# Performance work log

Measured on AMD Instinct MI355X. Metric: run time of the kernel, lower is better.

The kernel has to match this reference:

```python
import jax, jax.numpy as jnp
import numpy as np

D_MODEL = 1024
N_HEADS = 16
D_K = D_MODEL // N_HEADS


def setup_inputs() -> dict:
    key = jax.random.key(0)
    kx, kq, kk, kv, ko = jax.random.split(key, 5)
    s = 1.0 / np.sqrt(D_MODEL)
    return {
        "x": jax.random.normal(kx, (4, 2048, D_MODEL), dtype=jnp.float32),
        "W_q": jax.random.normal(kq, (D_MODEL, D_MODEL), dtype=jnp.float32) * s,
        "W_k": jax.random.normal(kk, (D_MODEL, D_MODEL), dtype=jnp.float32) * s,
        "W_v": jax.random.normal(kv, (D_MODEL, D_MODEL), dtype=jnp.float32) * s,
        "W_o": jax.random.normal(ko, (D_MODEL, D_MODEL), dtype=jnp.float32) * s,
    }


def reference(x, W_q, W_k, W_v, W_o):
    B, S, _ = x.shape
    # torch nn.Linear computes x @ W.T; our W_* stored as [out, in]-equivalent square,
    # use plain x @ W (equivalent parameterization for a random weight).
    def split_heads(t):  # [B,S,D] -> [B,H,S,d_k]
        return t.reshape(B, S, N_HEADS, D_K).transpose(0, 2, 1, 3)

    Q = split_heads(x @ W_q)
    K = split_heads(x @ W_k)
    V = split_heads(x @ W_v)
    scale = 1.0 / np.sqrt(D_K).astype(np.float32)
    scores = jnp.einsum('bhqd,bhkd->bhqk', Q, K) * scale  # [B,H,S,S]
    causal_mask = jnp.tril(jnp.ones((S, S), dtype=bool))  # True = keep
    scores = jnp.where(causal_mask, scores, jnp.float32(-jnp.inf))
    attn = jax.nn.softmax(scores, axis=-1)
    out = jnp.einsum('bhqk,bhkd->bhqd', attn, V)  # [B,H,S,d_k]
    out = out.transpose(0, 2, 1, 3).reshape(B, S, D_MODEL)
    return out @ W_o
```

## Files before the change

kernel.cpp:

```cpp
#include <hip/hip_runtime.h>
#include <hip/hip_bf16.h>
#include <stdint.h>

#define B_SZ 4
#define SEQ 2048
#define DM 1024
#define NH 16
#define DK 64
#define BH (B_SZ * NH)
#define M_TOT (B_SZ * SEQ)

typedef unsigned short u16;
typedef u16 u16x8 __attribute__((ext_vector_type(8)));
typedef __bf16 bf16x8 __attribute__((ext_vector_type(8)));
typedef float f32x4 __attribute__((ext_vector_type(4)));

__device__ __forceinline__ u16 f2bf(float f) {
    return __builtin_bit_cast(u16, (__bf16)f);
}

__device__ __forceinline__ u16 f2bf_trunc(float f) {
    union { float f; uint32_t u; } v; v.f = f;
    return (u16)(v.u >> 16);
}

__device__ __forceinline__ f32x4 mfma16(u16x8 a, u16x8 b, f32x4 c) {
    return __builtin_amdgcn_mfma_f32_16x16x32_bf16(
        __builtin_bit_cast(bf16x8, a), __builtin_bit_cast(bf16x8, b), c, 0, 0, 0);
}

__device__ __forceinline__ void gload16_lds(const void* g, void* l) {
    __builtin_amdgcn_global_load_lds(
        (const __attribute__((address_space(1))) void*)(uintptr_t)g,
        (__attribute__((address_space(3))) void*)(uintptr_t)l, 16, 0, 0);
}

__global__ void cvt_bf16_kernel(const float* __restrict__ in, u16* __restrict__ out, int n4) {
    int i = blockIdx.x * blockDim.x + threadIdx.x;
    if (i < n4) {
        float4 v = ((const float4*)in)[i];
        ushort4 o;
        o.x = f2bf(v.x); o.y = f2bf(v.y); o.z = f2bf(v.z); o.w = f2bf(v.w);
        ((ushort4*)out)[i] = o;
    }
}

__global__ void transpose_w_kernel(const float* __restrict__ W0, const float* __restrict__ W1,
                                   u16* __restrict__ Wt) {
    __shared__ u16 tile[32][33];
    int bx = blockIdx.x, by = blockIdx.y, z = blockIdx.z;
    const float* W = z ? W1 : W0;
    u16* Wd = Wt + (size_t)z * DM * DM;
    int t = threadIdx.x;
    for (int i = 0; i < 4; i++) {
        int idx = t + i * 256;
        int r = idx >> 5, c = idx & 31;
        tile[r][c] = f2bf(W[(by * 32 + r) * DM + bx * 32 + c]);
    }
    __syncthreads();
    for (int i = 0; i < 4; i++) {
        int idx = t + i * 256;
        int r2 = idx >> 5, c2 = idx & 31;
        Wd[(bx * 32 + r2) * DM + by * 32 + c2] = tile[c2][r2];
    }
}

template <int AFP32, int MODE>
__global__ __launch_bounds__(256, 3) void gemm128(
    const void* __restrict__ Ain, const u16* __restrict__ Bt,
    void* __restrict__ C0p, void* __restrict__ C1p, float scale0) {
    __shared__ u16 As[128][32];
    __shared__ u16 Bs[128][32];
    const int K = DM;
    int m0 = blockIdx.x * 128;
    int n0 = blockIdx.y * 128;
    int tid = threadIdx.x;
    int lane = tid & 63, wave = tid >> 6;
    int quad = lane >> 4, l15 = lane & 15;
    int wm = wave >> 1, wn = wave & 1;

    f32x4 acc[4][4];
    for (int i = 0; i < 4; i++)
        for (int j = 0; j < 4; j++) acc[i][j] = f32x4{0.f, 0.f, 0.f, 0.f};

    int rS = lane >> 2;
    int cS = (lane & 3) * 8;

    for (int k0 = 0; k0 < K; k0 += 32) {
        __syncthreads();
        if (AFP32) {
            const float* A = (const float*)Ain;
            for (int i = 0; i < 4; i++) {
                int idx = tid + i * 256;
                int r = idx >> 3, c = (idx & 7) * 4;
                float4 v = *(const float4*)(&A[(size_t)(m0 + r) * K + k0 + c]);
                ushort4 o;
                o.x = f2bf(v.x); o.y = f2bf(v.y); o.z = f2bf(v.z); o.w = f2bf(v.w);
                *(ushort4*)(&As[r][c]) = o;
            }
        } else {
            const u16* A = (const u16*)Ain;
            const u16* ga = &A[(size_t)(m0 + wave * 32 + rS) * K + k0 + cS];
            gload16_lds(ga, &As[wave * 32][0]);
            gload16_lds(ga + (size_t)16 * K, &As[wave * 32 + 16][0]);
        }
        {
            const u16* gb = &Bt[(size_t)(n0 + wave * 32 + rS) * K + k0 + cS];
            gload16_lds(gb, &Bs[wave * 32][0]);
            gload16_lds(gb + (size_t)16 * K, &Bs[wave * 32 + 16][0]);
        }
        __syncthreads();
        u16x8 af[4], bfv[4];
        for (int mt = 0; mt < 4; mt++)
            af[mt] = *(const u16x8*)(&As[wm * 64 + mt * 16 + l15][quad * 8]);
        for (int nt = 0; nt < 4; nt++)
            bfv[nt] = *(const u16x8*)(&Bs[wn * 64 + nt * 16 + l15][quad * 8]);
        for (int mt = 0; mt < 4; mt++)
            for (int nt = 0; nt < 4; nt++)
                acc[mt][nt] = mfma16(af[mt], bfv[nt], acc[mt][nt]);
    }

    if constexpr (MODE == 2) {
        __shared__ u16 Ct[4][64][68];
        #pragma unroll
        for (int mt = 0; mt < 4; mt++)
            #pragma unroll
            for (int nt = 0; nt < 4; nt++)
                #pragma unroll
                for (int r = 0; r < 4; r++) {
                    int mp = mt * 16 + quad * 4 + r;
                    int np = nt * 16 + l15;
                    Ct[wave][np][mp] = f2bf(acc[mt][nt][r]);
                }
        __syncthreads();
        int bb = m0 >> 11;
        int hh = (n0 + wn * 64) >> 6;
        int s_base = (m0 & 2047) + wm * 64;
        u16* Cv = (u16*)C0p;
        #pragma unroll
        for (int c = 0; c < 8; c++) {
            int np = (lane >> 3) + c * 8;
            int mp = (lane & 7) * 8;
            ushort4 lo = *(const ushort4*)(&Ct[wave][np][mp]);
            ushort4 hi = *(const ushort4*)(&Ct[wave][np][mp + 4]);
            u16x8 v;
            v[0] = lo.x; v[1] = lo.y; v[2] = lo.z; v[3] = lo.w;
            v[4] = hi.x; v[5] = hi.y; v[6] = hi.z; v[7] = hi.w;
            size_t addr = ((size_t)(bb * NH + hh) * DK + np) * SEQ + s_base + mp;
            *(u16x8*)(&Cv[addr]) = v;
        }
    } else {
        for (int mt = 0; mt < 4; mt++)
            for (int nt = 0; nt < 4; nt++)
                for (int r = 0; r < 4; r++) {
                    int m = m0 + wm * 64 + mt * 16 + quad * 4 + r;
                    int n = n0 + wn * 64 + nt * 16 + l15;
                    float v = acc[mt][nt][r];
                    if (MODE == 0) {
                        v *= (n < 1024) ? scale0 : 1.0f;
                        u16* C = (n < 1024) ? (u16*)C0p : (u16*)C1p;
                        int ne = n & 1023;
                        int b = m >> 11, s = m & 2047;
                        int h = ne >> 6, d = ne & 63;
                        C[(((size_t)(b * NH + h) * SEQ) + s) * DK + d] = f2bf(v);
                    } else {
                        ((float*)C0p)[(size_t)m * DM + n] = v;
                    }
                }
    }
}

__global__ __launch_bounds__(256, 3) void attn_kernel(
    const u16* __restrict__ Qb, const u16* __restrict__ Kb,
    const u16* __restrict__ Vtb, u16* __restrict__ AOb) {
    __shared__ u16 Kl[2][64][64];
    __shared__ u16 Vl[2][64][64];
    __shared__ u16 Pl[4][32][64];

    int bh = blockIdx.x;
    int qs = 15 - blockIdx.y;
    int q0 = qs * 128;
    int tid = threadIdx.x, lane = tid & 63, wave = tid >> 6;
    int quad = lane >> 4, l15 = lane & 15;
    int b = bh >> 4, h = bh & 15;

    const u16* Qg = Qb + (size_t)bh * SEQ * DK;
    const u16* Kg = Kb + (size_t)bh * SEQ * DK;
    const u16* Vg = Vtb + (size_t)bh * DK * SEQ;

    int rw = lane >> 3;
    int gsw = (lane & 7) ^ rw;
    int sw8 = l15 & 7;
    u16* Pw = &Pl[wave][0][0];

    u16x8 aq[2][2];
    for (int g = 0; g < 2; g++)
        for (int kc = 0; kc < 2; kc++)
            aq[g][kc] = *(const u16x8*)(
                &Qg[(size_t)(q0 + wave * 32 + g * 16 + l15) * DK + kc * 32 + quad * 8]);

    float lsum[2][4];
    f32x4 O[2][4];
    for (int g = 0; g < 2; g++)
        for (int r = 0; r < 4; r++) lsum[g][r] = 0.f;
    for (int g = 0; g < 2; g++)
        for (int nt = 0; nt < 4; nt++) O[g][nt] = f32x4{0.f, 0.f, 0.f, 0.f};

    {
        const u16* gk = &Kg[(size_t)(wave * 16 + rw) * DK + gsw * 8];
        gload16_lds(gk, &Kl[0][wave * 16][0]);
        gload16_lds(gk + 8 * DK, &Kl[0][wave * 16 + 8][0]);
        const u16* gv = &Vg[(size_t)(wave * 16 + rw) * SEQ + gsw * 8];
        gload16_lds(gv, &Vl[0][wave * 16][0]);
        gload16_lds(gv + 8 * SEQ, &Vl[0][wave * 16 + 8][0]);
    }
    __syncthreads();

    int nkt = 2 * qs + 2;
    int lastkt = 2 * qs + (wave >> 1);
    int buf = 0;
    for (int kt = 0; kt < nkt; kt++) {
        if (kt + 1 < nkt) {
            int k0n = (kt + 1) * 64;
            const u16* gk = &Kg[(size_t)(k0n + wave * 16 + rw) * DK + gsw * 8];
            gload16_lds(gk, &Kl[buf ^ 1][wave * 16][0]);
            gload16_lds(gk + 8 * DK, &Kl[buf ^ 1][wave * 16 + 8][0]);
            const u16* gv = &Vg[(size_t)(wave * 16 + rw) * SEQ + k0n + gsw * 8];
            gload16_lds(gv, &Vl[buf ^ 1][wave * 16][0]);
            gload16_lds(gv + 8 * SEQ, &Vl[buf ^ 1][wave * 16 + 8][0]);
        }

        if (kt <= lastkt) {
            bool diag = (kt == lastkt);
            f32x4 sc[2][4];
            __builtin_amdgcn_s_setprio(1);
            #pragma unroll
            for (int nt = 0; nt < 4; nt++) {
                const u16* kr = &Kl[buf][nt * 16 + l15][0];
                u16x8 b0 = *(const u16x8*)(kr + (quad ^ sw8) * 8);
                u16x8 b1 = *(const u16x8*)(kr + ((4 + quad) ^ sw8) * 8);
                #pragma unroll
                for (int g = 0; g < 2; g++) {
                    f32x4 z = f32x4{0.f, 0.f, 0.f, 0.f};
                    z = mfma16(aq[g][0], b0, z);
                    z = mfma16(aq[g][1], b1, z);
                    sc[g][nt] = z;
                }
            }
            __builtin_amdgcn_s_setprio(0);
            #pragma unroll
            for (int g = 0; g < 2; g++) {
                if (diag) {
                    #pragma unroll
                    for (int nt = 0; nt < 4; nt++)
                        #pragma unroll
                        for (int r = 0; r < 4; r++) {
                            int qq = q0 + wave * 32 + g * 16 + quad * 4 + r;
                            int kk = kt * 64 + nt * 16 + l15;
                            float e = exp2f(sc[g][nt][r]);
                            float pv = (kk <= qq) ? e : 0.f;
                            sc[g][nt][r] = pv;
                            lsum[g][r] += pv;
                        }
                } else {
                    #pragma unroll
                    for (int nt = 0; nt < 4; nt++)
                        #pragma unroll
                        for (int r = 0; r < 4; r++) {
                            float pv = exp2f(sc[g][nt][r]);
                            sc[g][nt][r] = pv;
                            lsum[g][r] += pv;
                        }
                }
                #pragma unroll
                for (int nt = 0; nt < 4; nt++)
                    #pragma unroll
                    for (int r = 0; r < 4; r++) {
                        int prow = g * 16 + quad * 4 + r;
                        int pcol = nt * 16 + l15;
                        int scol = (((pcol >> 3) ^ (prow & 7)) << 3) | (pcol & 7);
                        Pw[prow * 64 + scol] = f2bf_trunc(sc[g][nt][r]);
                    }
            }
            u16x8 ap[2][2];
            #pragma unroll
            for (int g = 0; g < 2; g++)
                #pragma unroll
                for (int kc = 0; kc < 2; kc++)
                    ap[g][kc] = *(const u16x8*)(
                        &Pw[(g * 16 + l15) * 64 + (((kc * 4 + quad) ^ sw8) << 3)]);
            __builtin_amdgcn_s_setprio(1);
            #pragma unroll
            for (int nt = 0; nt < 4; nt++) {
                const u16* vr = &Vl[buf][nt * 16 + l15][0];
                u16x8 b0 = *(const u16x8*)(vr + (quad ^ sw8) * 8);
                u16x8 b1 = *(const u16x8*)(vr + ((4 + quad) ^ sw8) * 8);
                #pragma unroll
                for (int g = 0; g < 2; g++) {
                    O[g][nt] = mfma16(ap[g][0], b0, O[g][nt]);
                    O[g][nt] = mfma16(ap[g][1], b1, O[g][nt]);
                }
            }
            __builtin_amdgcn_s_setprio(0);
        }
        __syncthreads();
        buf ^= 1;
    }

    #pragma unroll
    for (int g = 0; g < 2; g++)
        #pragma unroll
        for (int r = 0; r < 4; r++) {
            float s = lsum[g][r];
            for (int off = 1; off < 16; off <<= 1) s += __shfl_xor(s, off, 64);
            float inv = 1.0f / s;
            int q = q0 + wave * 32 + g * 16 + quad * 4 + r;
            #pragma unroll
            for (int nt = 0; nt < 4; nt++) {
                int d = nt * 16 + l15;
                AOb[((size_t)(b * SEQ + q)) * DM + h * DK + d] = f2bf(O[g][nt][r] * inv);
            }
        }
}

extern "C" void kernel_launch(void* const* d_in, const int* in_sizes, int n_in,
                              void* d_out, int out_size, void* d_ws, size_t ws_size,
                              hipStream_t stream) {
    const float* x = (const float*)d_in[0];
    const float* Wq = (const float*)d_in[1];
    const float* Wk = (const float*)d_in[2];
    const float* Wv = (const float*)d_in[3];
    const float* Wo = (const float*)d_in[4];
    float* out = (float*)d_out;

    const size_t HALF = (size_t)M_TOT * DM * 2;
    char* S0 = (char*)d_ws;
    char* S1 = (char*)d_ws + HALF;
    char* D0 = (char*)d_out;
    char* D1 = (char*)d_out + HALF;

    u16* xb  = (u16*)S0;
    u16* Qb  = (u16*)S1;
    u16* Kb  = (u16*)D1;
    u16* Vt  = (u16*)D0;
    u16* AOb = (u16*)S0;
    u16* wqk = (u16*)D0;
    u16* wvt = (u16*)S0;
    u16* wot = (u16*)S1;

    const float cscale = 0.125f * 1.44269504088896f;
    dim3 tg2(32, 32, 2);
    dim3 tg1(32, 32, 1);
    dim3 gg(M_TOT / 128, DM / 128);

    int n4 = M_TOT * DM / 4;
    cvt_bf16_kernel<<<n4 / 256, 256, 0, stream>>>(x, xb, n4);

    transpose_w_kernel<<<tg2, 256, 0, stream>>>(Wq, Wk, wqk);
    dim3 gqk(M_TOT / 128, 2048 / 128);
    gemm128<0, 0><<<gqk, 256, 0, stream>>>(xb, wqk, (void*)Qb, (void*)Kb, cscale);

    transpose_w_kernel<<<tg1, 256, 0, stream>>>(Wv, Wv, wvt);
    gemm128<1, 2><<<gg, 256, 0, stream>>>(x, wvt, (void*)Vt, (void*)Vt, 1.0f);

    dim3 ag(BH, 16);
    attn_kernel<<<ag, 256, 0, stream>>>(Qb, Kb, Vt, AOb);

    transpose_w_kernel<<<tg1, 256, 0, stream>>>(Wo, Wo, wot);
    gemm128<0, 1><<<gg, 256, 0, stream>>>(AOb, wot, (void*)out, (void*)out, 1.0f);
}
```

Baseline: 268.5 us.

## Double-buffer GEMM tiles with async LDS loads, XOR swizzle and grid swizzle

Rewrites the projection GEMM main loop to use a K-tile of 64 with two LDS buffers, prefetching two tiles ahead through direct global-to-LDS loads gated by vmcnt waits. The fp32 A operand is now staged raw into LDS and converted to bf16 on read, rather than converted through registers during the copy. XOR swizzles are added to the LDS layout to avoid bank conflicts, block indices are remapped for L2 locality, and MFMA sections get raised priority. The larger LDS footprint lowers occupancy (launch bounds drop to 1 or 2 blocks), and the hand-written waitcnt values must match the exact number of issued loads.

```diff
diff --git a/kernel.cpp b/kernel.cpp
--- a/kernel.cpp
+++ b/kernel.cpp
@@ -65,59 +65,140 @@
     }
 }
 
+template <int AFP32>
+__device__ __forceinline__ void stage_tile(const void* Ag, const u16* Btg,
+                                           char* Apart, char* Bpart, int buf, int kst,
+                                           int m0, int n0, int wave, int lane) {
+    const int K = DM;
+    {
+        int rw = lane >> 3, slot = lane & 7;
+        int gsw = slot ^ rw;
+        u16* Bb = (u16*)(Bpart + buf * (128 * 64 * 2));
+        #pragma unroll
+        for (int c = 0; c < 4; c++) {
+            int r0 = wave * 32 + c * 8;
+            gload16_lds(Btg + (size_t)(n0 + r0 + rw) * K + kst + gsw * 8, Bb + r0 * 64);
+        }
+    }
+    if constexpr (AFP32) {
+        int rw = lane >> 4, slot = lane & 15;
+        float* Ab = (float*)(Apart + buf * (128 * 64 * 4));
+        const float* Af = (const float*)Ag;
+        #pragma unroll
+        for (int c = 0; c < 8; c++) {
+            int r0 = wave * 32 + c * 4;
+            int gsw = slot ^ ((c * 4 + rw) & 15);
+            gload16_lds(Af + (size_t)(m0 + r0 + rw) * K + kst + gsw * 4, Ab + r0 * 64);
+        }
+    } else {
+        int rw = lane >> 3, slot = lane & 7;
+        int gsw = slot ^ rw;
+        u16* Ab = (u16*)(Apart + buf * (128 * 64 * 2));
+        const u16* Au = (const u16*)Ag;
+        #pragma unroll
+        for (int c = 0; c < 4; c++) {
+            int r0 = wave * 32 + c * 8;
+            gload16_lds(Au + (size_t)(m0 + r0 + rw) * K + kst + gsw * 8, Ab + r0 * 64);
+        }
+    }
+}
+
 template <int AFP32, int MODE>
-__global__ __launch_bounds__(256, 3) void gemm128(
+__global__ __launch_bounds__(256, AFP32 ? 1 : 2) void gemm128(
     const void* __restrict__ Ain, const u16* __restrict__ Bt,
     void* __restrict__ C0p, void* __restrict__ C1p, float scale0) {
-    __shared__ u16 As[128][32];
-    __shared__ u16 Bs[128][32];
-    const int K = DM;
-    int m0 = blockIdx.x * 128;
-    int n0 = blockIdx.y * 128;
+    constexpr int ABY = AFP32 ? 128 * 64 * 4 : 128 * 64 * 2;
+    constexpr int BBY = 128 * 64 * 2;
+    constexpr int NT = DM / 64;
+    __shared__ __align__(16) char smem[2 * ABY + 2 * BBY];
+    char* Apart = smem;
+    char* Bpart = smem + 2 * ABY;
+
+    int gm = gridDim.x;
+    int lin = blockIdx.x + blockIdx.y * gm;
+    int cpx = (gm * gridDim.y) >> 3;
+    int swz = (lin & 7) * cpx + (lin >> 3);
+    int m0 = (swz % gm) * 128;
+    int n0 = (swz / gm) * 128;
+
     int tid = threadIdx.x;
     int lane = tid & 63, wave = tid >> 6;
     int quad = lane >> 4, l15 = lane & 15;
     int wm = wave >> 1, wn = wave & 1;
 
     f32x4 acc[4][4];
+    #pragma unroll
     for (int i = 0; i < 4; i++)
+        #pragma unroll
         for (int j = 0; j < 4; j++) acc[i][j] = f32x4{0.f, 0.f, 0.f, 0.f};
 
-    int rS = lane >> 2;
-    int cS = (lane & 3) * 8;
-
-    for (int k0 = 0; k0 < K; k0 += 32) {
-        __syncthreads();
-        if (AFP32) {
-            const float* A = (const float*)Ain;
-            for (int i = 0; i < 4; i++) {
-                int idx = tid + i * 256;
-                int r = idx >> 3, c = (idx & 7) * 4;
-                float4 v = *(const float4*)(&A[(size_t)(m0 + r) * K + k0 + c]);
-                ushort4 o;
-                o.x = f2bf(v.x); o.y = f2bf(v.y); o.z = f2bf(v.z); o.w = f2bf(v.w);
-                *(ushort4*)(&As[r][c]) = o;
+    stage_tile<AFP32>(Ain, Bt, Apart, Bpart, 0, 0, m0, n0, wave, lane);
+    stage_tile<AFP32>(Ain, Bt, Apart, Bpart, 1, 64, m0, n0, wave, lane);
+
+    for (int t = 0; t < NT; ++t) {
+        int buf = t & 1;
+        if constexpr (AFP32)
+            asm volatile("s_waitcnt vmcnt(12)" ::: "memory");
+        else
+            asm volatile("s_waitcnt vmcnt(8)" ::: "memory");
+        __builtin_amdgcn_s_barrier();
+
+        u16x8 afr[4][2], bfr[4][2];
+        {
+            const u16* Bb = (const u16*)(Bpart + buf * BBY);
+            #pragma unroll
+            for (int nt = 0; nt < 4; nt++) {
+                const u16* rp = Bb + (wn * 64 + nt * 16 + l15) * 64;
+                int sw = l15 & 7;
+                bfr[nt][0] = *(const u16x8*)(rp + ((quad ^ sw) << 3));
+                bfr[nt][1] = *(const u16x8*)(rp + (((4 + quad) ^ sw) << 3));
+            }
+        }
+        if constexpr (AFP32) {
+            const float* Ab = (const float*)(Apart + buf * ABY);
+            #pragma unroll
+            for (int mt = 0; mt < 4; mt++) {
+                const float* rp = Ab + (wm * 64 + mt * 16 + l15) * 64;
+                #pragma unroll
+                for (int ks = 0; ks < 2; ks++) {
+                    int g0 = ks * 8 + quad * 2;
+                    f32x4 v0 = *(const f32x4*)(rp + ((g0 ^ l15) << 2));
+                    f32x4 v1 = *(const f32x4*)(rp + (((g0 + 1) ^ l15) << 2));
+                    u16x8 tt;
+                    tt[0] = f2bf(v0[0]); tt[1] = f2bf(v0[1]);
+                    tt[2] = f2bf(v0[2]); tt[3] = f2bf(v0[3]);
+                    tt[4] = f2bf(v1[0]); tt[5] = f2bf(v1[1]);
+                    tt[6] = f2bf(v1[2]); tt[7] = f2bf(v1[3]);
+                    afr[mt][ks] = tt;
+                }
             }
         } else {
-            const u16* A = (const u16*)Ain;
-            const u16* ga = &A[(size_t)(m0 + wave * 32 + rS) * K + k0 + cS];
-            gload16_lds(ga, &As[wave * 32][0]);
-            gload16_lds(ga + (size_t)16 * K, &As[wave * 32 + 16][0]);
-        }
-        {
-            const u16* gb = &Bt[(size_t)(n0 + wave * 32 + rS) * K + k0 + cS];
-            gload16_lds(gb, &Bs[wave * 32][0]);
-            gload16_lds(gb + (size_t)16 * K, &Bs[wave * 32 + 16][0]);
-        }
-        __syncthreads();
-        u16x8 af[4], bfv[4];
+            const u16* Ab = (const u16*)(Apart + buf * ABY);
+            #pragma unroll
+            for (int mt = 0; mt < 4; mt++) {
+                const u16* rp = Ab + (wm * 64 + mt * 16 + l15) * 64;
+                int sw = l15 & 7;
+                afr[mt][0] = *(const u16x8*)(rp + ((quad ^ sw) << 3));
+                afr[mt][1] = *(const u16x8*)(rp + (((4 + quad) ^ sw) << 3));
+            }
+        }
+        asm volatile("s_waitcnt lgkmcnt(0)" ::: "memory");
+        __builtin_amdgcn_sched_barrier(0);
+        __builtin_amdgcn_s_barrier();
+
+        int t2 = t + 2;
+        if (t2 > NT - 1) t2 = NT - 1;
+        stage_tile<AFP32>(Ain, Bt, Apart, Bpart, buf, t2 * 64, m0, n0, wave, lane);
+
+        __builtin_amdgcn_s_setprio(1);
+        #pragma unroll
         for (int mt = 0; mt < 4; mt++)
-            af[mt] = *(const u16x8*)(&As[wm * 64 + mt * 16 + l15][quad * 8]);
-        for (int nt = 0; nt < 4; nt++)
-            bfv[nt] = *(const u16x8*)(&Bs[wn * 64 + nt * 16 + l15][quad * 8]);
-        for (int mt = 0; mt < 4; mt++)
-            for (int nt = 0; nt < 4; nt++)
-                acc[mt][nt] = mfma16(af[mt], bfv[nt], acc[mt][nt]);
+            #pragma unroll
+            for (int nt = 0; nt < 4; nt++) {
+                acc[mt][nt] = mfma16(afr[mt][0], bfr[nt][0], acc[mt][nt]);
+                acc[mt][nt] = mfma16(afr[mt][1], bfr[nt][1], acc[mt][nt]);
+            }
+        __builtin_amdgcn_s_setprio(0);
     }
 
     if constexpr (MODE == 2) {
@@ -150,8 +231,11 @@
             *(u16x8*)(&Cv[addr]) = v;
         }
     } else {
+        #pragma unroll
         for (int mt = 0; mt < 4; mt++)
+            #pragma unroll
             for (int nt = 0; nt < 4; nt++)
+                #pragma unroll
                 for (int r = 0; r < 4; r++) {
                     int m = m0 + wm * 64 + mt * 16 + quad * 4 + r;
                     int n = n0 + wn * 64 + nt * 16 + l15;
```

New measurement: 277.9 us. 1.03x slower.

## Add double-buffered 256x128 GEMM with XOR-swizzled LDS for QK and output projections

Applied to the files above, without the earlier changes.

Replaces the 128x128 single-buffered GEMM used for the QK and output projections with a 512-thread 256x128 tile kernel. It uses a BK=64 double-buffered global-to-LDS pipeline, XOR-swizzled LDS rows to avoid bank conflicts, grouped block ordering for L2 reuse and raised wave priority around the MFMA loop. The V projection keeps the old design in a separate specialized kernel. The aim is to hide memory latency and raise MFMA utilization, at the cost of more LDS per block and lower occupancy.

```diff
diff --git a/kernel.cpp b/kernel.cpp
--- a/kernel.cpp
+++ b/kernel.cpp
@@ -65,10 +65,117 @@
     }
 }
 
-template <int AFP32, int MODE>
-__global__ __launch_bounds__(256, 3) void gemm128(
-    const void* __restrict__ Ain, const u16* __restrict__ Bt,
+template <int MODE>
+__global__ __launch_bounds__(512, 2) void gemm256(
+    const u16* __restrict__ Ain, const u16* __restrict__ Bt,
     void* __restrict__ C0p, void* __restrict__ C1p, float scale0) {
+    constexpr int NT = DM / 64;
+    __shared__ __align__(16) u16 As[2 * 256 * 64];
+    __shared__ __align__(16) u16 Bs[2 * 128 * 64];
+
+    int gm = gridDim.x;
+    int lin = blockIdx.x + blockIdx.y * gm;
+    int cpx = (gm * gridDim.y) >> 3;
+    int swz = (lin & 7) * cpx + (lin >> 3);
+    int m0 = (swz % gm) * 256;
+    int n0 = (swz / gm) * 128;
+
+    int tid = threadIdx.x;
+    int lane = tid & 63, wave = tid >> 6;
+    int quad = lane >> 4, l15 = lane & 15;
+    int wm = wave >> 1, wn = wave & 1;
+
+    int rw = lane >> 3;
+    int gsw = (lane & 7) ^ rw;
+
+    f32x4 acc[4][4];
+    #pragma unroll
+    for (int i = 0; i < 4; i++)
+        #pragma unroll
+        for (int j = 0; j < 4; j++) acc[i][j] = f32x4{0.f, 0.f, 0.f, 0.f};
+
+    auto stage = [&](int buf, int kst) {
+        const u16* ga = Ain + (size_t)(m0 + wave * 32 + rw) * DM + kst + gsw * 8;
+        u16* la = As + buf * (256 * 64) + (wave * 32) * 64;
+        #pragma unroll
+        for (int c = 0; c < 4; c++)
+            gload16_lds(ga + (size_t)(c * 8) * DM, la + c * 8 * 64);
+        const u16* gb = Bt + (size_t)(n0 + wave * 16 + rw) * DM + kst + gsw * 8;
+        u16* lb = Bs + buf * (128 * 64) + (wave * 16) * 64;
+        gload16_lds(gb, lb);
+        gload16_lds(gb + (size_t)8 * DM, lb + 8 * 64);
+    };
+
+    stage(0, 0);
+    stage(1, 64);
+
+    int sw = l15 & 7;
+    for (int t = 0; t < NT; ++t) {
+        int buf = t & 1;
+        asm volatile("s_waitcnt vmcnt(6)" ::: "memory");
+        __builtin_amdgcn_s_barrier();
+
+        u16x8 afr[4][2], bfr[4][2];
+        {
+            const u16* Ab = As + buf * (256 * 64);
+            #pragma unroll
+            for (int mt = 0; mt < 4; mt++) {
+                const u16* rp = Ab + (wm * 64 + mt * 16 + l15) * 64;
+                afr[mt][0] = *(const u16x8*)(rp + ((quad ^ sw) << 3));
+                afr[mt][1] = *(const u16x8*)(rp + (((4 + quad) ^ sw) << 3));
+            }
+            const u16* Bb = Bs + buf * (128 * 64);
+            #pragma unroll
+            for (int nt = 0; nt < 4; nt++) {
+                const u16* rp = Bb + (wn * 64 + nt * 16 + l15) * 64;
+                bfr[nt][0] = *(const u16x8*)(rp + ((quad ^ sw) << 3));
+                bfr[nt][1] = *(const u16x8*)(rp + (((4 + quad) ^ sw) << 3));
+            }
+        }
+        asm volatile("s_waitcnt lgkmcnt(0)" ::: "memory");
+        __builtin_amdgcn_sched_barrier(0);
+        __builtin_amdgcn_s_barrier();
+
+        int t2 = t + 2;
+        if (t2 > NT - 1) t2 = NT - 1;
+        stage(buf, t2 * 64);
+
+        __builtin_amdgcn_s_setprio(1);
+        #pragma unroll
+        for (int mt = 0; mt < 4; mt++)
+            #pragma unroll
+            for (int nt = 0; nt < 4; nt++) {
+                acc[mt][nt] = mfma16(afr[mt][0], bfr[nt][0], acc[mt][nt]);
+                acc[mt][nt] = mfma16(afr[mt][1], bfr[nt][1], acc[mt][nt]);
+            }
+        __builtin_amdgcn_s_setprio(0);
+    }
+
+    #pragma unroll
+    for (int mt = 0; mt < 4; mt++)
+        #pragma unroll
+        for (int nt = 0; nt < 4; nt++)
+            #pragma unroll
+            for (int r = 0; r < 4; r++) {
+                int m = m0 + wm * 64 + mt * 16 + quad * 4 + r;
+                int n = n0 + wn * 64 + nt * 16 + l15;
+                float v = acc[mt][nt][r];
+                if (MODE == 0) {
+                    v *= (n < 1024) ? scale0 : 1.0f;
+                    u16* C = (n < 1024) ? (u16*)C0p : (u16*)C1p;
+                    int ne = n & 1023;
+                    int b = m >> 11, s = m & 2047;
+                    int h = ne >> 6, d = ne & 63;
+                    C[(((size_t)(b * NH + h) * SEQ) + s) * DK + d] = f2bf(v);
+                } else {
+                    ((float*)C0p)[(size_t)m * DM + n] = v;
+                }
+            }
+}
+
+__global__ __launch_bounds__(256, 2) void gemm_v(
+    const float* __restrict__ Ain, const u16* __restrict__ Bt,
+    u16* __restrict__ C0p) {
     __shared__ u16 As[128][32];
     __shared__ u16 Bs[128][32];
     const int K = DM;
@@ -88,21 +195,13 @@
 
     for (int k0 = 0; k0 < K; k0 += 32) {
         __syncthreads();
-        if (AFP32) {
-            const float* A = (const float*)Ain;
-            for (int i = 0; i < 4; i++) {
-                int idx = tid + i * 256;
-                int r = idx >> 3, c = (idx & 7) * 4;
-                float4 v = *(const float4*)(&A[(size_t)(m0 + r) * K + k0 + c]);
-                ushort4 o;
-                o.x = f2bf(v.x); o.y = f2bf(v.y); o.z = f2bf(v.z); o.w = f2bf(v.w);
-                *(ushort4*)(&As[r][c]) = o;
-            }
-        } else {
-            const u16* A = (const u16*)Ain;
-            const u16* ga = &A[(size_t)(m0 + wave * 32 + rS) * K + k0 + cS];
-            gload16_lds(ga, &As[wave * 32][0]);
-            gload16_lds(ga + (size_t)16 * K, &As[wave * 32 + 16][0]);
+        for (int i = 0; i < 4; i++) {
+            int idx = tid + i * 256;
+            int r = idx >> 3, c = (idx & 7) * 4;
+            float4 v = *(const float4*)(&Ain[(size_t)(m0 + r) * K + k0 + c]);
+            ushort4 o;
+            o.x = f2bf(v.x); o.y = f2bf(v.y); o.z = f2bf(v.z); o.w = f2bf(v.w);
+            *(ushort4*)(&As[r][c]) = o;
         }
         {
             const u16* gb = &Bt[(size_t)(n0 + wave * 32 + rS) * K + k0 + cS];
@@ -120,53 +219,32 @@
                 acc[mt][nt] = mfma16(af[mt], bfv[nt], acc[mt][nt]);
     }
 
-    if constexpr (MODE == 2) {
-        __shared__ u16 Ct[4][64][68];
-        #pragma unroll
-        for (int mt = 0; mt < 4; mt++)
-            #pragma unroll
-            for (int nt = 0; nt < 4; nt++)
-                #pragma unroll
-                for (int r = 0; r < 4; r++) {
-                    int mp = mt * 16 + quad * 4 + r;
-                    int np = nt * 16 + l15;
-                    Ct[wave][np][mp] = f2bf(acc[mt][nt][r]);
-                }
-        __syncthreads();
-        int bb = m0 >> 11;
-        int hh = (n0 + wn * 64) >> 6;
-        int s_base = (m0 & 2047) + wm * 64;
-        u16* Cv = (u16*)C0p;
-        #pragma unroll
-        for (int c = 0; c < 8; c++) {
-            int np = (lane >> 3) + c * 8;
-            int mp = (lane & 7) * 8;
-            ushort4 lo = *(const ushort4*)(&Ct[wave][np][mp]);
-            ushort4 hi = *(const ushort4*)(&Ct[wave][np][mp + 4]);
-            u16x8 v;
-            v[0] = lo.x; v[1] = lo.y; v[2] = lo.z; v[3] = lo.w;
-            v[4] = hi.x; v[5] = hi.y; v[6] = hi.z; v[7] = hi.w;
-            size_t addr = ((size_t)(bb * NH + hh) * DK + np) * SEQ + s_base + mp;
-            *(u16x8*)(&Cv[addr]) = v;
-        }
-    } else {
-        for (int mt = 0; mt < 4; mt++)
-            for (int nt = 0; nt < 4; nt++)
-                for (int r = 0; r < 4; r++) {
-                    int m = m0 + wm * 64 + mt * 16 + quad * 4 + r;
-                    int n = n0 + wn * 64 + nt * 16 + l15;
-                    float v = acc[mt][nt][r];
-                    if (MODE == 0) {
-                        v *= (n < 1024) ? scale0 : 1.0f;
-                        u16* C = (n < 1024) ? (u16*)C0p : (u16*)C1p;
-                        int ne = n & 1023;
-                        int b = m >> 11, s = m & 2047;
-                        int h = ne >> 6, d = ne & 63;
-                        C[(((size_t)(b * NH + h) * SEQ) + s) * DK + d] = f2bf(v);
-                    } else {
-                        ((float*)C0p)[(size_t)m * DM + n] = v;
-                    }
-                }
+    __shared__ u16 Ct[4][64][68];
+    #pragma unroll
+    for (int mt = 0; mt < 4; mt++)
+        #pragma unroll
+        for (int nt = 0; nt < 4; nt++)
+            #pragma unroll
+            for (int r = 0; r < 4; r++) {
+                int mp = mt * 16 + quad * 4 + r;
+                int np = nt * 16 + l15;
+                Ct[wave][np][mp] = f2bf(acc[mt][nt][r]);
+            }
+    __syncthreads();
+    int bb = m0 >> 11;
+    int hh = (n0 + wn * 64) >> 6;
+    int s_base = (m0 & 2047) + wm * 64;
+    #pragma unroll
+    for (int c = 0; c < 8; c++) {
+        int np = (lane >> 3) + c * 8;
+        int mp = (lane & 7) * 8;
+        ushort4 lo = *(const ushort4*)(&Ct[wave][np][mp]);
+        ushort4 hi = *(const ushort4*)(&Ct[wave][np][mp + 4]);
+        u16x8 v;
+        v[0] = lo.x; v[1] = lo.y; v[2] = lo.z; v[3] = lo.w;
+        v[4] = hi.x; v[5] = hi.y; v[6] = hi.z; v[7] = hi.w;
+        size_t addr = ((size_t)(bb * NH + hh) * DK + np) * SEQ + s_base + mp;
+        *(u16x8*)(&C0p[addr]) = v;
     }
 }
 
@@ -351,21 +429,22 @@
     const float cscale = 0.125f * 1.44269504088896f;
     dim3 tg2(32, 32, 2);
     dim3 tg1(32, 32, 1);
-    dim3 gg(M_TOT / 128, DM / 128);
 
     int n4 = M_TOT * DM / 4;
     cvt_bf16_kernel<<<n4 / 256, 256, 0, stream>>>(x, xb, n4);
 
     transpose_w_kernel<<<tg2, 256, 0, stream>>>(Wq, Wk, wqk);
-    dim3 gqk(M_TOT / 128, 2048 / 128);
-    gemm128<0, 0><<<gqk, 256, 0, stream>>>(xb, wqk, (void*)Qb, (void*)Kb, cscale);
+    dim3 gqk(M_TOT / 256, 2048 / 128);
+    gemm256<0><<<gqk, 512, 0, stream>>>(xb, wqk, (void*)Qb, (void*)Kb, cscale);
 
     transpose_w_kernel<<<tg1, 256, 0, stream>>>(Wv, Wv, wvt);
-    gemm128<1, 2><<<gg, 256, 0, stream>>>(x, wvt, (void*)Vt, (void*)Vt, 1.0f);
+    dim3 gv(M_TOT / 128, DM / 128);
+    gemm_v<<<gv, 256, 0, stream>>>(x, wvt, Vt);
 
     dim3 ag(BH, 16);
     attn_kernel<<<ag, 256, 0, stream>>>(Qb, Kb, Vt, AOb);
 
     transpose_w_kernel<<<tg1, 256, 0, stream>>>(Wo, Wo, wot);
-    gemm128<0, 1><<<gg, 256, 0, stream>>>(AOb, wot, (void*)out, (void*)out, 1.0f);
-}
+    dim3 go(M_TOT / 256, DM / 128);
+    gemm256<1><<<go, 512, 0, stream>>>(AOb, wot, (void*)out, (void*)out, 1.0f);
+}
```

Measured after the change: 270.5 us. Within noise of the previous version (+0.8%).
